# Kernel optimization log

Measured on AMD Instinct MI355X. Metric: run time of the kernel, lower is better.

## Reference

```python
import jax, jax.numpy as jnp
import numpy as np

BLOCK_SIZE = 3
SOBEL_PAD = 1  # sobel_size // 2
BLOCK_PAD = BLOCK_SIZE // 2

_SOBEL_X = jnp.array([[-1.0, 0.0, 1.0], [-2.0, 0.0, 2.0], [-1.0, 0.0, 1.0]], dtype=jnp.float32)[None, None]
_SOBEL_Y = jnp.array([[-1.0, -2.0, -1.0], [0.0, 0.0, 0.0], [1.0, 2.0, 1.0]], dtype=jnp.float32)[None, None]
_SUM_K = jnp.ones((1, 1, BLOCK_SIZE, BLOCK_SIZE), dtype=jnp.float32)


def _pad_replicate(x, p):
    return jnp.pad(x, ((0, 0), (0, 0), (p, p), (p, p)), mode='edge')


def _conv(x, k):
    return jax.lax.conv_general_dilated(
        x, k, window_strides=(1, 1), padding='VALID',
        dimension_numbers=('NCHW', 'OIHW', 'NCHW'))


def setup_inputs() -> dict:
    key = jax.random.key(0)
    image = jax.random.uniform(key, (8, 1, 1080, 1920), dtype=jnp.float32) * 255.0
    return {"image": image}


def reference(image) -> jnp.ndarray:
    img = image.astype(jnp.float32)
    img_p = _pad_replicate(img, SOBEL_PAD)
    Ix = _conv(img_p, _SOBEL_X)
    Iy = _conv(img_p, _SOBEL_Y)
    Ixx = Ix * Ix
    Iyy = Iy * Iy
    Ixy = Ix * Iy
    sum_Ixx = _conv(_pad_replicate(Ixx, BLOCK_PAD), _SUM_K)
    sum_Iyy = _conv(_pad_replicate(Iyy, BLOCK_PAD), _SUM_K)
    sum_Ixy = _conv(_pad_replicate(Ixy, BLOCK_PAD), _SUM_K)
    half_trace = (sum_Ixx + sum_Iyy) * 0.5
    diff_half = (sum_Ixx - sum_Iyy) * 0.5
    sqrt_disc = jnp.sqrt(diff_half * diff_half + sum_Ixy * sum_Ixy + 1e-10)
    lambda_min = half_trace - sqrt_disc
    return jnp.clip(lambda_min, 0.0)
```

## Files before the change

kernel.cpp:

```cpp
#include <hip/hip_runtime.h>

typedef float v2f __attribute__((ext_vector_type(2)));
typedef float v4f __attribute__((ext_vector_type(4)));

#define IMG_H 1080
#define IMG_W 1920
#define NBATCH 8
#define LSTRIP 9
#define BROWS (4*LSTRIP)
#define NK (LSTRIP+4)


static __device__ __forceinline__ v2f vfma2(v2f a, v2f b, v2f c) {
    return __builtin_elementwise_fma(a, b, c);
}
static __device__ __forceinline__ float bperm(int addr, float v) {
    return __int_as_float(__builtin_amdgcn_ds_bpermute(addr, __float_as_int(v)));
}

__global__ __launch_bounds__(256, 4)
void shi_tomasi_kernel(const float* __restrict__ img, float* __restrict__ out) {
    const int cg    = threadIdx.x & 63;
    const int strip = threadIdx.x >> 6;
    const int bx    = blockIdx.x;
    const int c0    = bx * 240 + cg * 4;
    const int c0l   = min(c0, IMG_W - 4);
    const int s0    = blockIdx.y * BROWS + strip * LSTRIP;
    const float* g  = img + (size_t)blockIdx.z * (IMG_H * IMG_W);
    float* outb     = out + (size_t)blockIdx.z * (IMG_H * IMG_W);

    const bool eL     = (c0 == 0);
    const bool eR     = (c0 == IMG_W - 4);
    const bool hload  = (cg == 0) && (bx > 0);
    const bool doSt   = (cg < 60);
    const int  aLft   = 4 * (cg - 1);
    const int  aRgt   = 4 * (cg + 1);
    const bool topFix = (s0 == 0);
    const bool botFix = (s0 + LSTRIP == IMG_H);

    v4f Zr[4];
    v2f Hr[4] = {};
    v2f hdR[3][3], hsR[3][3];
    float hfd[3], hfs[3];
    v2f hxx[3][2], hyy[3][2], hxy[3][2];

    auto issue = [&](int k) {
        int lr = s0 - 2 + k;
        lr = max(0, min(IMG_H - 1, lr));
        const float* rowp = g + (size_t)lr * IMG_W;
        Zr[k % 4] = *(const v4f*)(rowp + c0l);
        if (hload) Hr[k % 4] = *(const v2f*)(rowp + (c0 - 2));
    };

    issue(0); issue(1); issue(2);

    const v2f two = {2.0f, 2.0f};

    #pragma unroll
    for (int k = 0; k < NK; ++k) {
        if (k + 3 < NK) issue(k + 3);

        {
            const v4f Z = Zr[k % 4];
            const float zl0 = bperm(aLft, Z.z), zl1 = bperm(aLft, Z.w);
            const float zr0 = bperm(aRgt, Z.x), zr1 = bperm(aRgt, Z.y);
            v2f Z0 = v2f{zl0, zl1};
            if (cg == 0) Z0 = eL ? v2f{Z.x, Z.x} : Hr[k % 4];
            const v2f Z1 = v2f{Z.x, Z.y};
            const v2f Z2 = v2f{Z.z, Z.w};
            v2f Z3 = v2f{zr0, zr1};
            if (eR) Z3 = v2f{Z.w, Z.w};

            const v2f Sab = v2f{Z0.y, Z1.x};
            const v2f Sbc = v2f{Z1.y, Z2.x};
            const v2f Scd = v2f{Z2.y, Z3.x};
            v2f* hd = hdR[k % 3];
            v2f* hs = hsR[k % 3];
            hd[0] = Z1 - Z0; hd[1] = Z2 - Z1; hd[2] = Z3 - Z2;
            hs[0] = vfma2(Sab, two, Z0) + Z1;
            hs[1] = vfma2(Sbc, two, Z1) + Z2;
            hs[2] = vfma2(Scd, two, Z2) + Z3;
            hfd[k % 3] = eR ? (Z2.y - Z2.x) : (Z1.y - Z1.x);
            hfs[k % 3] = eR ? (Z2.x + 3.0f * Z2.y) : (3.0f * Z1.x + Z1.y);
        }

        if (k >= 2) {
            const int rr = k - 2;
            const int sm = rr % 3, sz = (rr + 1) % 3, sp = (rr + 2) % 3;

            v2f Ixp[3], Iyp[3];
            #pragma unroll
            for (int j = 0; j < 3; ++j) {
                Ixp[j] = vfma2(hdR[sz][j], two, hdR[sm][j]) + hdR[sp][j];
                Iyp[j] = hsR[sp][j] - hsR[sm][j];
            }
            const float ixf = hfd[sm] + 2.0f * hfd[sz] + hfd[sp];
            const float iyf = hfs[sp] - hfs[sm];
            if (eL) { Ixp[0].x = ixf; Iyp[0].x = iyf; }
            if (eR) { Ixp[2].y = ixf; Iyp[2].y = iyf; }

            v2f xx[3], yy[3], xy[3];
            #pragma unroll
            for (int j = 0; j < 3; ++j) {
                xx[j] = Ixp[j] * Ixp[j];
                yy[j] = Iyp[j] * Iyp[j];
                xy[j] = Ixp[j] * Iyp[j];
            }
            {
                v2f* hx = hxx[rr % 3];
                v2f* hy = hyy[rr % 3];
                v2f* hz = hxy[rr % 3];
                hx[0] = xx[0] + v2f{xx[0].y, xx[1].x} + xx[1];
                hx[1] = xx[1] + v2f{xx[1].y, xx[2].x} + xx[2];
                hy[0] = yy[0] + v2f{yy[0].y, yy[1].x} + yy[1];
                hy[1] = yy[1] + v2f{yy[1].y, yy[2].x} + yy[2];
                hz[0] = xy[0] + v2f{xy[0].y, xy[1].x} + xy[1];
                hz[1] = xy[1] + v2f{xy[1].y, xy[2].x} + xy[2];
            }
            if (rr == 1 && topFix) {
                #pragma unroll
                for (int q = 0; q < 2; ++q) {
                    hxx[0][q] = hxx[1][q]; hyy[0][q] = hyy[1][q]; hxy[0][q] = hxy[1][q];
                }
            }
            if (rr == LSTRIP + 1 && botFix) {
                #pragma unroll
                for (int q = 0; q < 2; ++q) {
                    hxx[rr % 3][q] = hxx[(rr - 1) % 3][q];
                    hyy[rr % 3][q] = hyy[(rr - 1) % 3][q];
                    hxy[rr % 3][q] = hxy[(rr - 1) % 3][q];
                }
            }

            if (rr >= 2) {
                const int a = (rr - 2) % 3, b2 = (rr - 1) % 3, c = rr % 3;
                float rv[4];
                #pragma unroll
                for (int q = 0; q < 2; ++q) {
                    const v2f sxx = hxx[a][q] + hxx[b2][q] + hxx[c][q];
                    const v2f syy = hyy[a][q] + hyy[b2][q] + hyy[c][q];
                    const v2f sxy = hxy[a][q] + hxy[b2][q] + hxy[c][q];
                    const v2f S = sxx + syy;
                    const v2f D = sxx - syy;
                    const v2f E = sxy + sxy;
                    const v2f disc = vfma2(D, D, vfma2(E, E, v2f{4e-10f, 4e-10f}));
                    const v2f qv = {__builtin_sqrtf(disc.x), __builtin_sqrtf(disc.y)};
                    const v2f lam = (S - qv) * 0.5f;
                    rv[2 * q]     = fmaxf(lam.x, 0.0f);
                    rv[2 * q + 1] = fmaxf(lam.y, 0.0f);
                }
                if (doSt) {
                    float* orowp = outb + (size_t)(s0 + rr - 2) * IMG_W + c0;
                    *(v4f*)orowp = v4f{rv[0], rv[1], rv[2], rv[3]};
                }
            }
        }
    }
}

extern "C" void kernel_launch(void* const* d_in, const int* in_sizes, int n_in,
                              void* d_out, int out_size, void* d_ws, size_t ws_size,
                              hipStream_t stream) {
    const float* img = (const float*)d_in[0];
    float* out = (float*)d_out;
    dim3 grid(8, IMG_H / BROWS, NBATCH);
    shi_tomasi_kernel<<<grid, 256, 0, stream>>>(img, out);
}
```

Baseline: 120.1 us.

## Use halo lanes for neighbor columns and preload all strip rows

The column mapping is shifted so lanes 0-1 and 62-63 of each wavefront load halo columns. The per-row conditional halo load and lane-0 special case go away, and neighbours now come only through bpermute; those halo lanes skip the store. All NK row loads are also issued up front into registers instead of through a 3-deep rolling prefetch, with launch bounds lowered to 3 blocks per SIMD to allow the higher register use. This trades lower occupancy and a few redundant halo lanes for more memory-level parallelism and simpler control flow.

Result: no change. 118.0 us (-1.8%).

```diff
diff --git a/kernel.cpp b/kernel.cpp
--- a/kernel.cpp
+++ b/kernel.cpp
@@ -18,54 +18,48 @@
     return __int_as_float(__builtin_amdgcn_ds_bpermute(addr, __float_as_int(v)));
 }
 
-__global__ __launch_bounds__(256, 4)
+__global__ __launch_bounds__(256, 3)
 void shi_tomasi_kernel(const float* __restrict__ img, float* __restrict__ out) {
     const int cg    = threadIdx.x & 63;
     const int strip = threadIdx.x >> 6;
     const int bx    = blockIdx.x;
-    const int c0    = bx * 240 + cg * 4;
-    const int c0l   = min(c0, IMG_W - 4);
+    const int base  = bx * 240;
+    const int cl    = min(max(base - 8 + 4 * cg, 0), IMG_W - 4);
+    const int c0    = base + 4 * (cg - 2);
     const int s0    = blockIdx.y * BROWS + strip * LSTRIP;
     const float* g  = img + (size_t)blockIdx.z * (IMG_H * IMG_W);
     float* outb     = out + (size_t)blockIdx.z * (IMG_H * IMG_W);
 
-    const bool eL     = (c0 == 0);
-    const bool eR     = (c0 == IMG_W - 4);
-    const bool hload  = (cg == 0) && (bx > 0);
-    const bool doSt   = (cg < 60);
+    const bool eL     = (bx == 0) && (cg == 2);
+    const bool eR     = (bx == 7) && (cg == 61);
+    const bool doSt   = (cg >= 2) && (cg < 62);
     const int  aLft   = 4 * (cg - 1);
     const int  aRgt   = 4 * (cg + 1);
     const bool topFix = (s0 == 0);
     const bool botFix = (s0 + LSTRIP == IMG_H);
 
-    v4f Zr[4];
-    v2f Hr[4] = {};
+    v4f Zr[NK];
+    const float* lp = g + cl;
+    #pragma unroll
+    for (int k = 0; k < NK; ++k) {
+        int lr = s0 - 2 + k;
+        lr = max(0, min(IMG_H - 1, lr));
+        Zr[k] = *(const v4f*)(lp + (size_t)lr * IMG_W);
+    }
+
     v2f hdR[3][3], hsR[3][3];
     float hfd[3], hfs[3];
     v2f hxx[3][2], hyy[3][2], hxy[3][2];
-
-    auto issue = [&](int k) {
-        int lr = s0 - 2 + k;
-        lr = max(0, min(IMG_H - 1, lr));
-        const float* rowp = g + (size_t)lr * IMG_W;
-        Zr[k % 4] = *(const v4f*)(rowp + c0l);
-        if (hload) Hr[k % 4] = *(const v2f*)(rowp + (c0 - 2));
-    };
-
-    issue(0); issue(1); issue(2);
-
     const v2f two = {2.0f, 2.0f};
 
     #pragma unroll
     for (int k = 0; k < NK; ++k) {
-        if (k + 3 < NK) issue(k + 3);
-
         {
-            const v4f Z = Zr[k % 4];
+            const v4f Z = Zr[k];
             const float zl0 = bperm(aLft, Z.z), zl1 = bperm(aLft, Z.w);
             const float zr0 = bperm(aRgt, Z.x), zr1 = bperm(aRgt, Z.y);
             v2f Z0 = v2f{zl0, zl1};
-            if (cg == 0) Z0 = eL ? v2f{Z.x, Z.x} : Hr[k % 4];
+            if (eL) Z0 = v2f{Z.x, Z.x};
             const v2f Z1 = v2f{Z.x, Z.y};
             const v2f Z2 = v2f{Z.z, Z.w};
             v2f Z3 = v2f{zr0, zr1};
```
